# Performance work log

Hardware: AMD Instinct MI355X
Metric: run time of the kernel (lower is better)

The kernel has to match this reference:

```python
import jax, jax.numpy as jnp
import numpy as np

B, L, D, H = 32, 512, 512, 8


def setup_inputs() -> dict:
    key = jax.random.key(0)
    ks = jax.random.split(key, 6)
    s = 0.02
    return {
        "queries": jax.random.normal(ks[0], (B, L, D), jnp.float32),
        "keys": jax.random.normal(ks[1], (B, L, D), jnp.float32),
        "Wq": jax.random.normal(ks[2], (D, D), jnp.float32) * s,
        "bq": jnp.zeros((D,), jnp.float32),
        "Wk": jax.random.normal(ks[3], (D, D), jnp.float32) * s,
        "bk": jnp.zeros((D,), jnp.float32),
        "Wv": jax.random.normal(ks[4], (D, D), jnp.float32) * s,
        "bv": jnp.zeros((D,), jnp.float32),
        "causality": 1,
    }


def reference(queries, keys, Wq, bq, Wk, bk, Wv, bv, causality):
    b, lq, d = queries.shape
    lk = keys.shape[1]
    dh = d // H

    # torch Linear: x @ W.T + b
    Q = queries @ Wq.T + bq
    K = keys @ Wk.T + bk
    V = keys @ Wv.T + bv

    # chunk along feature dim then cat along batch == head-major [H, B, L, dh]
    def split_heads(x, l):
        return x.reshape(b, l, H, dh).transpose(2, 0, 1, 3)

    Qh = split_heads(Q, lq)
    Kh = split_heads(K, lk)
    Vh = split_heads(V, lk)

    scores = jnp.einsum('hbqd,hbkd->hbqk', Qh, Kh) / jnp.sqrt(jnp.asarray(dh, queries.dtype))

    # sign-based key padding mask: zero rows of `keys` get -inf scores
    key_mask = jnp.sign(jnp.sum(jnp.abs(keys), axis=-1))  # [B, Lk]
    scores = jnp.where(key_mask[None, :, None, :] == 0, -jnp.inf, scores)

    if causality:
        tril = jnp.tril(jnp.ones((lq, lk), dtype=bool))
        scores = jnp.where(tril[None, None, :, :], scores, -jnp.inf)

    w = jax.nn.softmax(scores, axis=-1)
    w = jnp.nan_to_num(w, nan=0.0, posinf=0.0, neginf=0.0)

    # sign-based query mask multiplied AFTER softmax
    query_mask = jnp.sign(jnp.sum(jnp.abs(queries), axis=-1))  # [B, Lq]
    w = w * query_mask[None, :, :, None]

    attention_weights = w.transpose(1, 0, 2, 3)  # [B, H, Lq, Lk]

    # dropout is identity in eval mode
    out = jnp.einsum('hbqk,hbkd->hbqd', w, Vh)          # [H, B, Lq, dh]
    out = out.transpose(1, 2, 0, 3).reshape(b, lq, d)    # head-major concat on feature dim
    return out, attention_weights
```

## Files before the change

### kernel.cpp

```cpp
#include <hip/hip_runtime.h>
#include <math.h>

typedef short short8 __attribute__((ext_vector_type(8)));
typedef short short4v __attribute__((ext_vector_type(4)));
typedef float float4v __attribute__((ext_vector_type(4)));

__device__ __forceinline__ short f2bf(float f) {
    union { float f; unsigned u; } v; v.f = f;
    unsigned r = (v.u + 0x7FFFu + ((v.u >> 16) & 1u)) >> 16;
    return (short)r;
}

__device__ __forceinline__ void async16(const short* g, short* l) {
    __builtin_amdgcn_global_load_lds(
        (const __attribute__((address_space(1))) unsigned*)g,
        (__attribute__((address_space(3))) unsigned*)l, 16, 0, 0);
}

__global__ __launch_bounds__(256) void cvt3_kernel(
    const float* __restrict__ w0, const float* __restrict__ w1, const float* __restrict__ w2,
    short* __restrict__ d0, short* __restrict__ d1, short* __restrict__ d2) {
    int i = blockIdx.x * blockDim.x + threadIdx.x;
    int sel = i >> 16;
    int j = i & 65535;
    const float* src = (sel == 0) ? w0 : (sel == 1) ? w1 : w2;
    short* dst       = (sel == 0) ? d0 : (sel == 1) ? d1 : d2;
    float4v v = ((const float4v*)src)[j];
    short4v o;
    o[0] = f2bf(v[0]); o[1] = f2bf(v[1]); o[2] = f2bf(v[2]); o[3] = f2bf(v[3]);
    ((short4v*)dst)[j] = o;
}

__global__ __launch_bounds__(256) void cvtmask_kernel(
    const float* __restrict__ q, const float* __restrict__ k,
    short* __restrict__ qb, short* __restrict__ kb,
    float* __restrict__ qm, float* __restrict__ km) {
    int tid = threadIdx.x;
    int lane = tid & 63, wv = tid >> 6;
    int row = blockIdx.x * 4 + wv;
    const float* src; short* dst; float* msk; int r;
    if (row < 16384) { src = q; dst = qb; msk = qm; r = row; }
    else             { src = k; dst = kb; msk = km; r = row - 16384; }
    const float4v* p = (const float4v*)(src + (size_t)r * 512);
    float4v a = p[lane];
    float4v b = p[lane + 64];
    short4v o1, o2;
    o1[0] = f2bf(a[0]); o1[1] = f2bf(a[1]); o1[2] = f2bf(a[2]); o1[3] = f2bf(a[3]);
    o2[0] = f2bf(b[0]); o2[1] = f2bf(b[1]); o2[2] = f2bf(b[2]); o2[3] = f2bf(b[3]);
    short4v* d4 = (short4v*)(dst + (size_t)r * 512);
    d4[lane] = o1;
    d4[lane + 64] = o2;
    float s = fabsf(a[0]) + fabsf(a[1]) + fabsf(a[2]) + fabsf(a[3])
            + fabsf(b[0]) + fabsf(b[1]) + fabsf(b[2]) + fabsf(b[3]);
    #pragma unroll
    for (int off = 1; off < 64; off <<= 1) s += __shfl_xor(s, off, 64);
    if (lane == 0) msk[r] = (s > 0.f) ? 1.f : 0.f;
}

__global__ __launch_bounds__(256) void proj_kernel(
    const short* __restrict__ Xq, const short* __restrict__ Xk,
    const short* __restrict__ Wqp, const short* __restrict__ Wkp, const short* __restrict__ Wvp,
    const float* __restrict__ bqp, const float* __restrict__ bkp, const float* __restrict__ bvp,
    short* __restrict__ Qo, short* __restrict__ Ko, short* __restrict__ Vo) {
    __shared__ short As[128 * 64];
    __shared__ short Bs[128 * 64];
    int z = blockIdx.z;
    const short* X    = (z == 0) ? Xq  : Xk;
    const short* W    = (z == 0) ? Wqp : (z == 1) ? Wkp : Wvp;
    const float* bias = (z == 0) ? bqp : (z == 1) ? bkp : bvp;
    short* out        = (z == 0) ? Qo  : (z == 1) ? Ko  : Vo;

    int tid = threadIdx.x;
    int lane = tid & 63, wv = tid >> 6;
    int col = lane & 15, quad = lane >> 4;
    int m0 = blockIdx.x * 128;
    int n0 = blockIdx.y * 128;
    int msub = (wv & 1) * 64, nsub = (wv >> 1) * 64;

    float4v acc[4][4];
    #pragma unroll
    for (int mt = 0; mt < 4; ++mt)
        #pragma unroll
        for (int nt = 0; nt < 4; ++nt) { acc[mt][nt][0]=0.f; acc[mt][nt][1]=0.f; acc[mt][nt][2]=0.f; acc[mt][nt][3]=0.f; }

    int rowS = tid >> 3;
    int seg  = tid & 7;
    const short* gA = X + (size_t)(m0 + rowS) * 512 + seg * 8;
    const short* gB = W + (size_t)(n0 + rowS) * 512 + seg * 8;
    short* lA = As + (size_t)tid * 8;
    short* lB = Bs + (size_t)tid * 8;

    for (int k0 = 0; k0 < 512; k0 += 64) {
        __syncthreads();
        #pragma unroll
        for (int j = 0; j < 4; ++j) {
            async16(gA + (size_t)(j * 32) * 512 + k0, lA + j * 2048);
            async16(gB + (size_t)(j * 32) * 512 + k0, lB + j * 2048);
        }
        __syncthreads();
        #pragma unroll
        for (int ksub = 0; ksub < 2; ++ksub) {
            short8 a[4], b[4];
            #pragma unroll
            for (int mt = 0; mt < 4; ++mt)
                a[mt] = *(const short8*)(As + (msub + mt * 16 + col) * 64 + ksub * 32 + quad * 8);
            #pragma unroll
            for (int nt = 0; nt < 4; ++nt)
                b[nt] = *(const short8*)(Bs + (nsub + nt * 16 + col) * 64 + ksub * 32 + quad * 8);
            #pragma unroll
            for (int mt = 0; mt < 4; ++mt)
                #pragma unroll
                for (int nt = 0; nt < 4; ++nt)
                    acc[mt][nt] = __builtin_amdgcn_mfma_f32_16x16x32_bf16(a[mt], b[nt], acc[mt][nt], 0, 0, 0);
        }
    }

    #pragma unroll
    for (int nt = 0; nt < 4; ++nt) {
        float bv = bias[n0 + nsub + nt * 16 + col];
        #pragma unroll
        for (int mt = 0; mt < 4; ++mt) {
            #pragma unroll
            for (int r = 0; r < 4; ++r) {
                int m = m0 + msub + mt * 16 + quad * 4 + r;
                out[(size_t)m * 512 + n0 + nsub + nt * 16 + col] = f2bf(acc[mt][nt][r] + bv);
            }
        }
    }
}

__global__ __launch_bounds__(256) void attn_kernel(
    const short* __restrict__ Q, const short* __restrict__ K, const short* __restrict__ V,
    const float* __restrict__ qmask, const float* __restrict__ kmask,
    const int* __restrict__ caus, float* __restrict__ out, float* __restrict__ aw) {
    __shared__ short vtb[2][64 * 72];
    __shared__ short wl[4 * 16 * 72];

    int tid = threadIdx.x;
    int lane = tid & 63, wv = tid >> 6;
    int col = lane & 15, quad = lane >> 4;
    int bh = blockIdx.x, qt = blockIdx.y;
    int b = bh >> 3, h = bh & 7;
    int q0 = qt * 64 + wv * 16;
    size_t rowbase = (size_t)b * 512;
    bool causal = (*caus) != 0;
    int lim = causal ? (qt * 4 + wv) : 31;
    int climit = causal ? qt : 7;

    short8 bQ0, bQ1;
    {
        const short* qp = Q + (rowbase + q0 + col) * 512 + h * 64 + quad * 8;
        bQ0 = *(const short8*)(qp);
        bQ1 = *(const short8*)(qp + 32);
    }

    const short* kp = K + (rowbase + col) * 512 + h * 64 + quad * 8;
    const float* kmp = kmask + b * 512;
    int qg = q0 + col;
    const float C = 0.125f * 1.44269504089f;

    float m = -INFINITY, l = 0.f;
    #pragma unroll
    for (int t = 0; t < 32; ++t) {
        if (t <= lim) {
            short8 aK0 = *(const short8*)(kp + (size_t)(t * 16) * 512);
            short8 aK1 = *(const short8*)(kp + (size_t)(t * 16) * 512 + 32);
            float4v s; s[0]=0.f; s[1]=0.f; s[2]=0.f; s[3]=0.f;
            s = __builtin_amdgcn_mfma_f32_16x16x32_bf16(aK0, bQ0, s, 0, 0, 0);
            s = __builtin_amdgcn_mfma_f32_16x16x32_bf16(aK1, bQ1, s, 0, 0, 0);
            int kb = t * 16 + quad * 4;
            float4v km4 = *(const float4v*)(kmp + kb);
            float e0, e1, e2, e3, tmax;
            e0 = ((km4[0] != 0.f) && (!causal || (kb + 0 <= qg))) ? s[0] * C : -INFINITY;
            e1 = ((km4[1] != 0.f) && (!causal || (kb + 1 <= qg))) ? s[1] * C : -INFINITY;
            e2 = ((km4[2] != 0.f) && (!causal || (kb + 2 <= qg))) ? s[2] * C : -INFINITY;
            e3 = ((km4[3] != 0.f) && (!causal || (kb + 3 <= qg))) ? s[3] * C : -INFINITY;
            tmax = fmaxf(fmaxf(e0, e1), fmaxf(e2, e3));
            float nm = fmaxf(m, tmax);
            float f = (m == -INFINITY) ? 0.f : exp2f(m - nm);
            float ls = 0.f;
            ls += (e0 == -INFINITY) ? 0.f : exp2f(e0 - nm);
            ls += (e1 == -INFINITY) ? 0.f : exp2f(e1 - nm);
            ls += (e2 == -INFINITY) ? 0.f : exp2f(e2 - nm);
            ls += (e3 == -INFINITY) ? 0.f : exp2f(e3 - nm);
            l = l * f + ls;
            m = nm;
        }
    }
    #pragma unroll
    for (int off = 16; off <= 32; off <<= 1) {
        float mo = __shfl_xor(m, off, 64);
        float lo = __shfl_xor(l, off, 64);
        float M = fmaxf(m, mo);
        float fa = (m  == -INFINITY) ? 0.f : exp2f(m - M);
        float fb = (mo == -INFINITY) ? 0.f : exp2f(mo - M);
        l = l * fa + lo * fb;
        m = M;
    }
    float qmv = qmask[b * 512 + qg];
    float inv = (l > 0.f) ? (qmv / l) : 0.f;

    int kk0 = tid >> 3, sgv = tid & 7;
    const short* vp = V + rowbase * 512 + h * 64 + sgv * 8;
    int lck0 = kk0 ^ (sgv << 3);
    int lck1 = (kk0 + 32) ^ (sgv << 3);
    short8 pva = *(const short8*)(vp + (size_t)(kk0) * 512);
    short8 pvb = *(const short8*)(vp + (size_t)(kk0 + 32) * 512);

    float4v O[4];
    #pragma unroll
    for (int nt = 0; nt < 4; ++nt) { O[nt][0]=0.f; O[nt][1]=0.f; O[nt][2]=0.f; O[nt][3]=0.f; }
    short* wlw = wl + wv * (16 * 72);
    float* awr = aw + ((size_t)b * 8 + h) * 512 * 512 + (size_t)qg * 512 + quad * 4;
    float4v z4; z4[0]=0.f; z4[1]=0.f; z4[2]=0.f; z4[3]=0.f;

    #pragma unroll
    for (int c = 0; c < 8; ++c) {
        if (c <= climit) {
            short* vb = &vtb[c & 1][0];
            #pragma unroll
            for (int j = 0; j < 8; ++j) vb[(sgv * 8 + j) * 72 + lck0] = pva[j];
            #pragma unroll
            for (int j = 0; j < 8; ++j) vb[(sgv * 8 + j) * 72 + lck1] = pvb[j];
            __syncthreads();
            if (c + 1 <= climit) {
                pva = *(const short8*)(vp + (size_t)((c + 1) * 64 + kk0) * 512);
                pvb = *(const short8*)(vp + (size_t)((c + 1) * 64 + kk0 + 32) * 512);
            }
            #pragma unroll
            for (int tl = 0; tl < 4; ++tl) {
                int t = c * 4 + tl;
                short4v w4;
                if (t <= lim) {
                    short8 aK0 = *(const short8*)(kp + (size_t)(t * 16) * 512);
                    short8 aK1 = *(const short8*)(kp + (size_t)(t * 16) * 512 + 32);
                    float4v s; s[0]=0.f; s[1]=0.f; s[2]=0.f; s[3]=0.f;
                    s = __builtin_amdgcn_mfma_f32_16x16x32_bf16(aK0, bQ0, s, 0, 0, 0);
                    s = __builtin_amdgcn_mfma_f32_16x16x32_bf16(aK1, bQ1, s, 0, 0, 0);
                    int kb = t * 16 + quad * 4;
                    float4v km4 = *(const float4v*)(kmp + kb);
                    float4v w;
                    #pragma unroll
                    for (int r = 0; r < 4; ++r) {
                        bool ok = (km4[r] != 0.f) && (!causal || (kb + r <= qg)) && (inv > 0.f);
                        float wvv = ok ? exp2f(s[r] * C - m) * inv : 0.f;
                        w[r] = wvv;
                        w4[r] = f2bf(wvv);
                    }
                    __builtin_nontemporal_store(w, (float4v*)(awr + t * 16));
                } else {
                    w4[0]=0; w4[1]=0; w4[2]=0; w4[3]=0;
                    __builtin_nontemporal_store(z4, (float4v*)(awr + t * 16));
                }
                *(short4v*)(wlw + col * 72 + tl * 16 + quad * 4) = w4;
            }
            #pragma unroll
            for (int sub = 0; sub < 2; ++sub) {
                short8 aW = *(const short8*)(wlw + col * 72 + sub * 32 + quad * 8);
                #pragma unroll
                for (int nt = 0; nt < 4; ++nt) {
                    int d = nt * 16 + col;
                    int cb = (sub * 32 + quad * 8) ^ (((d >> 3) & 7) << 3);
                    short8 bV = *(const short8*)(vb + d * 72 + cb);
                    O[nt] = __builtin_amdgcn_mfma_f32_16x16x32_bf16(aW, bV, O[nt], 0, 0, 0);
                }
            }
        } else {
            #pragma unroll
            for (int tl = 0; tl < 4; ++tl)
                __builtin_nontemporal_store(z4, (float4v*)(awr + (c * 4 + tl) * 16));
        }
    }

    #pragma unroll
    for (int nt = 0; nt < 4; ++nt) {
        #pragma unroll
        for (int r = 0; r < 4; ++r) {
            int qq = q0 + quad * 4 + r;
            __builtin_nontemporal_store(O[nt][r],
                out + (rowbase + qq) * 512 + h * 64 + nt * 16 + col);
        }
    }
}

extern "C" void kernel_launch(void* const* d_in, const int* in_sizes, int n_in,
                              void* d_out, int out_size, void* d_ws, size_t ws_size,
                              hipStream_t stream) {
    const float* queries = (const float*)d_in[0];
    const float* keys    = (const float*)d_in[1];
    const float* Wq      = (const float*)d_in[2];
    const float* bq      = (const float*)d_in[3];
    const float* Wk      = (const float*)d_in[4];
    const float* bk      = (const float*)d_in[5];
    const float* Wv      = (const float*)d_in[6];
    const float* bv      = (const float*)d_in[7];
    const int*   caus    = (const int*)d_in[8];

    const size_t NE = (size_t)16384 * 512;
    short* qbf = (short*)d_ws;
    short* kbf = qbf + NE;
    short* Qb  = kbf + NE;
    short* Kb  = Qb + NE;
    short* Vb  = Kb + NE;
    short* wqb = Vb + NE;
    short* wkb = wqb + 512 * 512;
    short* wvb = wkb + 512 * 512;
    float* qm  = (float*)(wvb + 512 * 512);
    float* km  = qm + 32 * 512;

    cvtmask_kernel<<<8192, 256, 0, stream>>>(queries, keys, qbf, kbf, qm, km);
    cvt3_kernel<<<768, 256, 0, stream>>>(Wq, Wk, Wv, wqb, wkb, wvb);
    dim3 pg(128, 4, 3);
    proj_kernel<<<pg, 256, 0, stream>>>(qbf, kbf, wqb, wkb, wvb, bq, bk, bv, Qb, Kb, Vb);
    float* outp = (float*)d_out;
    float* awp  = outp + 8388608;
    dim3 ag(256, 8);
    attn_kernel<<<ag, 256, 0, stream>>>(Qb, Kb, Vb, qm, km, caus, outp, awp);
}
```

Baseline: 500.9 us.

## Double-buffer projection GEMM LDS tiles and fold weight conversion into mask kernel

The projection GEMM now keeps two LDS buffers for the A and B tiles. The next k-slice is loaded asynchronously while MFMA runs on the current one, and one barrier per iteration is removed. Separately, the weight bf16 conversion is merged into the input conversion/mask kernel as extra blocks, which saves one kernel launch. The cost is doubled LDS use in the projection kernel (64KB), which can lower occupancy. The attention kernel, which likely dominates runtime, is unchanged.

Result: no change. 509.5 us (+1.7%).

```diff
diff --git a/kernel.cpp b/kernel.cpp
--- a/kernel.cpp
+++ b/kernel.cpp
@@ -17,25 +17,25 @@
         (__attribute__((address_space(3))) unsigned*)l, 16, 0, 0);
 }
 
-__global__ __launch_bounds__(256) void cvt3_kernel(
-    const float* __restrict__ w0, const float* __restrict__ w1, const float* __restrict__ w2,
-    short* __restrict__ d0, short* __restrict__ d1, short* __restrict__ d2) {
-    int i = blockIdx.x * blockDim.x + threadIdx.x;
-    int sel = i >> 16;
-    int j = i & 65535;
-    const float* src = (sel == 0) ? w0 : (sel == 1) ? w1 : w2;
-    short* dst       = (sel == 0) ? d0 : (sel == 1) ? d1 : d2;
-    float4v v = ((const float4v*)src)[j];
-    short4v o;
-    o[0] = f2bf(v[0]); o[1] = f2bf(v[1]); o[2] = f2bf(v[2]); o[3] = f2bf(v[3]);
-    ((short4v*)dst)[j] = o;
-}
-
 __global__ __launch_bounds__(256) void cvtmask_kernel(
     const float* __restrict__ q, const float* __restrict__ k,
     short* __restrict__ qb, short* __restrict__ kb,
-    float* __restrict__ qm, float* __restrict__ km) {
+    float* __restrict__ qm, float* __restrict__ km,
+    const float* __restrict__ w0, const float* __restrict__ w1, const float* __restrict__ w2,
+    short* __restrict__ d0, short* __restrict__ d1, short* __restrict__ d2) {
     int tid = threadIdx.x;
+    if (blockIdx.x >= 8192) {
+        int i = (blockIdx.x - 8192) * 256 + tid;
+        int sel = i >> 16;
+        int j = i & 65535;
+        const float* src = (sel == 0) ? w0 : (sel == 1) ? w1 : w2;
+        short* dst       = (sel == 0) ? d0 : (sel == 1) ? d1 : d2;
+        float4v v = ((const float4v*)src)[j];
+        short4v o;
+        o[0] = f2bf(v[0]); o[1] = f2bf(v[1]); o[2] = f2bf(v[2]); o[3] = f2bf(v[3]);
+        ((short4v*)dst)[j] = o;
+        return;
+    }
     int lane = tid & 63, wv = tid >> 6;
     int row = blockIdx.x * 4 + wv;
     const float* src; short* dst; float* msk; int r;
@@ -62,8 +62,8 @@
     const short* __restrict__ Wqp, const short* __restrict__ Wkp, const short* __restrict__ Wvp,
     const float* __restrict__ bqp, const float* __restrict__ bkp, const float* __restrict__ bvp,
     short* __restrict__ Qo, short* __restrict__ Ko, short* __restrict__ Vo) {
-    __shared__ short As[128 * 64];
-    __shared__ short Bs[128 * 64];
+    __shared__ short As[2][128 * 64];
+    __shared__ short Bs[2][128 * 64];
     int z = blockIdx.z;
     const short* X    = (z == 0) ? Xq  : Xk;
     const short* W    = (z == 0) ? Wqp : (z == 1) ? Wkp : Wvp;
@@ -87,26 +87,33 @@
     int seg  = tid & 7;
     const short* gA = X + (size_t)(m0 + rowS) * 512 + seg * 8;
     const short* gB = W + (size_t)(n0 + rowS) * 512 + seg * 8;
-    short* lA = As + (size_t)tid * 8;
-    short* lB = Bs + (size_t)tid * 8;
+
+    #pragma unroll
+    for (int j = 0; j < 4; ++j) {
+        async16(gA + (size_t)(j * 32) * 512, &As[0][0] + (size_t)tid * 8 + j * 2048);
+        async16(gB + (size_t)(j * 32) * 512, &Bs[0][0] + (size_t)tid * 8 + j * 2048);
+    }
 
     for (int k0 = 0; k0 < 512; k0 += 64) {
+        int cur = (k0 >> 6) & 1;
         __syncthreads();
-        #pragma unroll
-        for (int j = 0; j < 4; ++j) {
-            async16(gA + (size_t)(j * 32) * 512 + k0, lA + j * 2048);
-            async16(gB + (size_t)(j * 32) * 512 + k0, lB + j * 2048);
-        }
-        __syncthreads();
+        if (k0 + 64 < 512) {
+            int nxt = cur ^ 1;
+            #pragma unroll
+            for (int j = 0; j < 4; ++j) {
+                async16(gA + (size_t)(j * 32) * 512 + k0 + 64, &As[nxt][0] + (size_t)tid * 8 + j * 2048);
+                async16(gB + (size_t)(j * 32) * 512 + k0 + 64, &Bs[nxt][0] + (size_t)tid * 8 + j * 2048);
+            }
+        }
         #pragma unroll
         for (int ksub = 0; ksub < 2; ++ksub) {
             short8 a[4], b[4];
             #pragma unroll
             for (int mt = 0; mt < 4; ++mt)
-                a[mt] = *(const short8*)(As + (msub + mt * 16 + col) * 64 + ksub * 32 + quad * 8);
+                a[mt] = *(const short8*)(&As[cur][0] + (msub + mt * 16 + col) * 64 + ksub * 32 + quad * 8);
             #pragma unroll
             for (int nt = 0; nt < 4; ++nt)
-                b[nt] = *(const short8*)(Bs + (nsub + nt * 16 + col) * 64 + ksub * 32 + quad * 8);
+                b[nt] = *(const short8*)(&Bs[cur][0] + (nsub + nt * 16 + col) * 64 + ksub * 32 + quad * 8);
             #pragma unroll
             for (int mt = 0; mt < 4; ++mt)
                 #pragma unroll
@@ -308,8 +315,8 @@
     float* qm  = (float*)(wvb + 512 * 512);
     float* km  = qm + 32 * 512;
 
-    cvtmask_kernel<<<8192, 256, 0, stream>>>(queries, keys, qbf, kbf, qm, km);
-    cvt3_kernel<<<768, 256, 0, stream>>>(Wq, Wk, Wv, wqb, wkb, wvb);
+    cvtmask_kernel<<<8960, 256, 0, stream>>>(queries, keys, qbf, kbf, qm, km,
+                                             Wq, Wk, Wv, wqb, wkb, wvb);
     dim3 pg(128, 4, 3);
     proj_kernel<<<pg, 256, 0, stream>>>(qbf, kbf, wqb, wkb, wvb, bq, bk, bv, Qb, Kb, Vb);
     float* outp = (float*)d_out;
```
